# Kernel tuning notes

Hardware: AMD Instinct MI355X
Metric: run time of the kernel (lower is better)

The kernel has to match this reference:

```python
import jax, jax.numpy as jnp
import numpy as np
from jax import lax

NUM_PATCHES = 64   # FPS sample count K
PATCH_SIZE = 32    # KNN neighbors per patch


def setup_inputs() -> dict:
    key = jax.random.key(0)
    points = jax.random.normal(key, (16, 65536, 3), dtype=jnp.float32)
    return {"points": points}


def _fps(xyz, K):
    """Iterative farthest point sampling. xyz: [B,N,3] -> idx [B,K].
    Deterministic start at index 0 (reference for random_start_point)."""
    B, N, _ = xyz.shape
    start = jnp.zeros((B,), dtype=jnp.int32)
    min_d0 = jnp.full((B, N), jnp.finfo(xyz.dtype).max, xyz.dtype)

    def step(carry, _):
        min_d, last = carry
        last_pt = jnp.take_along_axis(xyz, last[:, None, None], axis=1)  # [B,1,3]
        d = jnp.sum((xyz - last_pt) ** 2, axis=-1)                       # [B,N]
        min_d = jnp.minimum(min_d, d)
        nxt = jnp.argmax(min_d, axis=1).astype(jnp.int32)
        return (min_d, nxt), last

    (_, _), idxs = lax.scan(step, (min_d0, start), None, length=K)  # [K,B]
    return jnp.transpose(idxs)  # [B,K]


def _knn_idx(centers, pts, K):
    """K nearest neighbors (sorted ascending by distance). centers [B,P,3], pts [B,N,3]."""
    c2 = jnp.sum(centers * centers, -1)[:, :, None]                 # [B,P,1]
    p2 = jnp.sum(pts * pts, -1)[:, None, :]                         # [B,1,N]
    d2 = c2 + p2 - 2.0 * jnp.einsum('bpc,bnc->bpn', centers, pts)   # [B,P,N]
    _, idx = lax.top_k(-d2, K)                                      # sorted nearest-first
    return idx


def reference(points):
    xyz = points[..., :3]
    fps_idx = _fps(xyz, NUM_PATCHES)                                  # [B,P]
    centers = jnp.take_along_axis(xyz, fps_idx[..., None], axis=1)    # [B,P,3]
    idx = _knn_idx(centers, xyz, PATCH_SIZE)                          # [B,P,K]
    patches = jax.vmap(lambda p, i: p[i])(points, idx)                # [B,P,K,C]
    patches = patches.at[..., :3].add(-centers[:, :, None, :])        # center xyz part
    return patches, centers
```

## Files before the change

### kernel.cpp

```cpp
#include <hip/hip_runtime.h>
#include <float.h>

#define BATCH 16
#define NPTS  65536
#define NP    64
#define PS    32
#define SLICES 8
#define SLICE_PTS (NPTS / SLICES)
#define CAP   192


__device__ __forceinline__ unsigned long long enc64(double d) {
    unsigned long long u = (unsigned long long)__double_as_longlong(d);
    return u ^ ((u >> 63) ? 0xFFFFFFFFFFFFFFFFull : 0x8000000000000000ull);
}
__device__ __forceinline__ unsigned enc32(float f) {
    unsigned u = __float_as_uint(f);
    return u ^ ((u >> 31) ? 0xFFFFFFFFu : 0x80000000u);
}
__device__ __forceinline__ float dec32(unsigned e) {
    unsigned u = (e & 0x80000000u) ? (e ^ 0x80000000u) : ~e;
    return __uint_as_float(u);
}

#define SENT 0xFFFFFFFFFFFFFFFFull

__global__ __launch_bounds__(256, 2)
void fps_kernel(const float* __restrict__ pts,
                float* __restrict__ centers,
                unsigned long long* __restrict__ slots)
{
#pragma clang fp contract(off)
    const int b  = blockIdx.x & 15;
    const int wg = blockIdx.x >> 4;
    const int t  = threadIdx.x;
    const float* __restrict__ P = pts + (size_t)b * NPTS * 3;

    float x[16], y[16], z[16];
    double md[16];
    const int gi0 = wg * 4096 + t;
#pragma unroll
    for (int k = 0; k < 16; ++k) {
        int i = gi0 + (k << 8);
        x[k] = P[3*i+0]; y[k] = P[3*i+1]; z[k] = P[3*i+2];
        md[k] = DBL_MAX;
    }

    double cx = (double)P[0], cy = (double)P[1], cz = (double)P[2];
    if (wg == 0 && t == 0) {
        float* c0 = centers + b * (NP*3);
        c0[0] = P[0]; c0[1] = P[1]; c0[2] = P[2];
    }

    __shared__ unsigned long long wbest[4];
    __shared__ unsigned long long skey[16];

    unsigned long long* slot_it = slots + (size_t)b * 63 * 16;

    for (int it = 0; it < NP - 1; ++it) {
        double bd = -1.0; int bi = 0;
#pragma unroll
        for (int k = 0; k < 16; ++k) {
            double dx = (double)x[k] - cx;
            double dy = (double)y[k] - cy;
            double dz = (double)z[k] - cz;
            double d  = (dx*dx + dy*dy) + dz*dz;
            double m  = fmin(md[k], d);
            md[k] = m;
            if (m > bd) { bd = m; bi = gi0 + (k << 8); }
        }
        unsigned long long db  = (unsigned long long)__double_as_longlong(bd);
        unsigned long long key = 0x8000000000000000ull
                               | (db & 0xFFFFFFFFFFFF0000ull)
                               | (unsigned long long)((~bi) & 0xFFFF);
#pragma unroll
        for (int off = 32; off > 0; off >>= 1) {
            unsigned long long o = __shfl_xor(key, off, 64);
            if (o > key) key = o;
        }
        if ((t & 63) == 0) wbest[t >> 6] = key;
        __syncthreads();
        if (t == 0) {
            unsigned long long k0 = wbest[0];
            if (wbest[1] > k0) k0 = wbest[1];
            if (wbest[2] > k0) k0 = wbest[2];
            if (wbest[3] > k0) k0 = wbest[3];
            __hip_atomic_store(slot_it + wg, k0, __ATOMIC_RELAXED, __HIP_MEMORY_SCOPE_AGENT);
        }
        if (t < 16) {
            unsigned long long v;
            v = __hip_atomic_load(slot_it + t, __ATOMIC_RELAXED, __HIP_MEMORY_SCOPE_AGENT);
            while (v == 0) {
                __builtin_amdgcn_s_sleep(1);
                v = __hip_atomic_load(slot_it + t, __ATOMIC_RELAXED, __HIP_MEMORY_SCOPE_AGENT);
            }
            skey[t] = v;
        }
        __syncthreads();
        unsigned long long bk = skey[0];
#pragma unroll
        for (int j = 1; j < 16; ++j) if (skey[j] > bk) bk = skey[j];
        int sel = (int)((~bk) & 0xFFFFull);
        cx = (double)P[3*sel+0]; cy = (double)P[3*sel+1]; cz = (double)P[3*sel+2];
        if (wg == 0 && t == 0) {
            float* c = centers + b*(NP*3) + (it+1)*3;
            c[0] = P[3*sel+0]; c[1] = P[3*sel+1]; c[2] = P[3*sel+2];
        }
        slot_it += 16;
    }
}

__global__ __launch_bounds__(256, 4)
void knn_pass(const float* __restrict__ pts,
              const float* __restrict__ centers,
              unsigned long long* __restrict__ gkeys)
{
    const int t    = threadIdx.x;
    const int lane = t & 63;
    const int wid  = t >> 6;
    const int b    = blockIdx.x & 15;
    const int w    = (blockIdx.x >> 4) & 15;
    const int s    = blockIdx.x >> 8;
    const float* __restrict__ P = pts + (size_t)b * NPTS * 3;
    const int sbase = s * SLICE_PTS;
    const float4* __restrict__ P4 = (const float4*)(P + 3 * sbase);

    float m2x[4], m2y[4], m2z[4], c2f[4];
#pragma unroll
    for (int g = 0; g < 4; ++g) {
        int c = b * NP + w * 4 + g;
        float cx = centers[3*c+0], cy = centers[3*c+1], cz = centers[3*c+2];
        c2f[g] = cx*cx + cy*cy + cz*cz;
        m2x[g] = -2.0f*cx; m2y[g] = -2.0f*cy; m2z[g] = -2.0f*cz;
    }

    union PoolKeys {
        unsigned pool[4][512];
        unsigned long long keys[4][CAP];
    };
    __shared__ PoolKeys pk;
    __shared__ float    theta4[4];
    __shared__ int      cnt4[4];
    __shared__ unsigned idxbuf[4][CAP];

    float s0[4], s1[4];
#pragma unroll
    for (int g = 0; g < 4; ++g) { s0[g] = FLT_MAX; s1[g] = FLT_MAX; }
    {
        float4 A = P4[3*t], B = P4[3*t+1], C = P4[3*t+2];
        for (int k = 0; k < SLICE_PTS/1024; ++k) {
            int vb = ((k+1) & 7)*768 + 3*t;
            float4 An = P4[vb], Bn = P4[vb+1], Cn = P4[vb+2];
            float qx[4] = {A.x, A.w, B.z, C.y};
            float qy[4] = {A.y, B.x, B.w, C.z};
            float qz[4] = {A.z, B.y, C.x, C.w};
#pragma unroll
            for (int j = 0; j < 4; ++j) {
                float px = qx[j], py = qy[j], pz = qz[j];
                float p2 = px*px + py*py + pz*pz;
#pragma unroll
                for (int g = 0; g < 4; ++g) {
                    float d2 = fmaf(m2x[g], px, fmaf(m2y[g], py, fmaf(m2z[g], pz, c2f[g]))) + p2;
                    s1[g] = __builtin_amdgcn_fmed3f(s0[g], s1[g], d2);
                    s0[g] = fminf(s0[g], d2);
                }
            }
            A = An; B = Bn; C = Cn;
        }
    }
#pragma unroll
    for (int g = 0; g < 4; ++g) {
        pk.pool[g][t]       = enc32(s0[g]);
        pk.pool[g][256 + t] = enc32(s1[g]);
    }
    if (t < 4) cnt4[t] = 0;
    __syncthreads();

    {
        const int g = wid;
        unsigned e[8];
#pragma unroll
        for (int j = 0; j < 8; ++j) e[j] = pk.pool[g][lane * 8 + j];
        unsigned ans = 0;
        for (int bit = 31; bit >= 0; --bit) {
            unsigned test = ans | ((1u << bit) - 1u);
            int cnt = 0;
#pragma unroll
            for (int j = 0; j < 8; ++j)
                cnt += (int)__popcll(__ballot(e[j] <= test));
            if (cnt < 32) ans |= (1u << bit);
        }
        if (lane == 0) theta4[g] = dec32(ans) + 4.0e-3f;
    }
    __syncthreads();
    float th[4];
#pragma unroll
    for (int g = 0; g < 4; ++g) th[g] = theta4[g];

    {
        float4 A = P4[3*t], B = P4[3*t+1], C = P4[3*t+2];
        for (int k = 0; k < SLICE_PTS/1024; ++k) {
            int vb = ((k+1) & 7)*768 + 3*t;
            float4 An = P4[vb], Bn = P4[vb+1], Cn = P4[vb+2];
            float qx[4] = {A.x, A.w, B.z, C.y};
            float qy[4] = {A.y, B.x, B.w, C.z};
            float qz[4] = {A.z, B.y, C.x, C.w};
            int ib = sbase + (k << 10) + (t << 2);
#pragma unroll
            for (int j = 0; j < 4; ++j) {
                float px = qx[j], py = qy[j], pz = qz[j];
                float p2 = px*px + py*py + pz*pz;
#pragma unroll
                for (int g = 0; g < 4; ++g) {
                    float d2 = fmaf(m2x[g], px, fmaf(m2y[g], py, fmaf(m2z[g], pz, c2f[g]))) + p2;
                    if (d2 <= th[g]) {
                        int pos = atomicAdd(&cnt4[g], 1);
                        if (pos < CAP) idxbuf[g][pos] = (unsigned)(ib + j);
                    }
                }
            }
            A = An; B = Bn; C = Cn;
        }
    }
    __syncthreads();

    {
        const int g = wid;
        int n = cnt4[g]; if (n > CAP) n = CAP;
        double cxd, cyd, czd, c2d;
        {
#pragma clang fp contract(off)
            cxd = -0.5*(double)m2x[g]; cyd = -0.5*(double)m2y[g]; czd = -0.5*(double)m2z[g];
            c2d = (cxd*cxd + cyd*cyd) + czd*czd;
        }
        unsigned long long rg[3];
#pragma unroll
        for (int j = 0; j < 3; ++j) {
            int p_ = lane + 64*j;
            if (p_ < n) {
                unsigned i = idxbuf[g][p_];
                double d2x;
                {
#pragma clang fp contract(off)
                    double px_ = (double)P[3*i+0];
                    double py_ = (double)P[3*i+1];
                    double pz_ = (double)P[3*i+2];
                    double p2_ = (px_*px_ + py_*py_) + pz_*pz_;
                    double dt_ = (cxd*px_ + cyd*py_) + czd*pz_;
                    d2x = (c2d + p2_) - 2.0*dt_;
                }
                rg[j] = (enc64(d2x) & 0xFFFFFFFFFFFF0000ull)
                      | (unsigned long long)(i & 0xFFFF);
                pk.keys[g][p_] = rg[j];
            } else rg[j] = SENT;
        }
        const int c = b * NP + w * 4 + g;
        int rank0 = 0, rank1 = 0, rank2 = 0;
        for (int p = 0; p < n; ++p) {
            unsigned long long kj = pk.keys[g][p];
            rank0 += (kj < rg[0]);
            rank1 += (kj < rg[1]);
            rank2 += (kj < rg[2]);
        }
        unsigned long long* gout = gkeys + ((size_t)c * SLICES + s) * PS;
        if (lane       < n && rank0 < PS) gout[rank0] = rg[0];
        if (lane + 64  < n && rank1 < PS) gout[rank1] = rg[1];
        if (lane + 128 < n && rank2 < PS) gout[rank2] = rg[2];
    }
}

__global__ __launch_bounds__(256, 4)
void knn_merge(const float* __restrict__ pts,
               const float* __restrict__ centers,
               const unsigned long long* __restrict__ gkeys,
               float* __restrict__ patches)
{
    const int lane = threadIdx.x & 63;
    const int wid  = threadIdx.x >> 6;
    const int b    = blockIdx.x & 15;
    const int grp  = blockIdx.x >> 4;
    const int c    = b * NP + grp * 4 + wid;
    const float* __restrict__ P = pts + (size_t)b * NPTS * 3;

    unsigned long long rg[4];
#pragma unroll
    for (int j = 0; j < 4; ++j)
        rg[j] = gkeys[(size_t)c * (SLICES*PS) + j*64 + lane];

    unsigned long long okey = SENT;
    for (int r = 0; r < PS; ++r) {
        unsigned long long mn = rg[0]; int mp = 0;
        if (rg[1] < mn) { mn = rg[1]; mp = 1; }
        if (rg[2] < mn) { mn = rg[2]; mp = 2; }
        if (rg[3] < mn) { mn = rg[3]; mp = 3; }
        unsigned long long wm = mn;
#pragma unroll
        for (int off = 32; off > 0; off >>= 1) {
            unsigned long long o = __shfl_xor(wm, off, 64);
            if (o < wm) wm = o;
        }
        if (wm == mn) {
            if (mp == 0) rg[0] = SENT;
            else if (mp == 1) rg[1] = SENT;
            else if (mp == 2) rg[2] = SENT;
            else rg[3] = SENT;
        }
        if (lane == r) okey = wm;
    }

    const float cx = centers[3*c+0], cy = centers[3*c+1], cz = centers[3*c+2];
    if (lane < PS) {
        int i = (int)(okey & 0xFFFFull);
        float* o = patches + (((size_t)c * PS) + lane) * 3;
        o[0] = P[3*i+0] - cx;
        o[1] = P[3*i+1] - cy;
        o[2] = P[3*i+2] - cz;
    }
}

extern "C" void kernel_launch(void* const* d_in, const int* in_sizes, int n_in,
                              void* d_out, int out_size, void* d_ws, size_t ws_size,
                              hipStream_t stream)
{
    const float* pts = (const float*)d_in[0];
    float* out      = (float*)d_out;
    float* patches  = out;
    float* centers  = out + (size_t)BATCH*NP*PS*3;

    unsigned long long* slots = (unsigned long long*)d_ws;
    unsigned long long* gkeys = (unsigned long long*)((char*)d_ws + 131072);

    (void)hipMemsetAsync(d_ws, 0, (size_t)BATCH * 63 * 16 * sizeof(unsigned long long), stream);
    fps_kernel<<<dim3(256), dim3(256), 0, stream>>>(pts, centers, slots);
    knn_pass<<<dim3(2048), dim3(256), 0, stream>>>(pts, centers, gkeys);
    knn_merge<<<dim3(256), dim3(256), 0, stream>>>(pts, centers, gkeys, patches);
}
```

Baseline: 224.0 us.

## Halve KNN slices and replace merge tournament with rank-based placement

Cuts the number of point slices per center from 8 to 4, so each knn_pass block scans twice as many points and the grid launches half as many blocks. The per-slice candidate cap grows to 256, and the exact double-precision ranking covers four keys per lane. The merge kernel drops the 32-round shuffle-min tournament and instead ranks 128 candidates by counting through shared memory, writing each top-32 key straight to its output position. The threshold pool is also read in a strided, lane-contiguous order. The trade is fewer blocks and less parallelism in the scan pass against a shorter merge and less candidate traffic.

```diff
diff --git a/kernel.cpp b/kernel.cpp
--- a/kernel.cpp
+++ b/kernel.cpp
@@ -5,9 +5,9 @@
 #define NPTS  65536
 #define NP    64
 #define PS    32
-#define SLICES 8
+#define SLICES 4
 #define SLICE_PTS (NPTS / SLICES)
-#define CAP   192
+#define CAP   256
 
 
 __device__ __forceinline__ unsigned long long enc64(double d) {
@@ -149,7 +149,7 @@
     {
         float4 A = P4[3*t], B = P4[3*t+1], C = P4[3*t+2];
         for (int k = 0; k < SLICE_PTS/1024; ++k) {
-            int vb = ((k+1) & 7)*768 + 3*t;
+            int vb = ((k+1) & 15)*768 + 3*t;
             float4 An = P4[vb], Bn = P4[vb+1], Cn = P4[vb+2];
             float qx[4] = {A.x, A.w, B.z, C.y};
             float qy[4] = {A.y, B.x, B.w, C.z};
@@ -180,7 +180,7 @@
         const int g = wid;
         unsigned e[8];
 #pragma unroll
-        for (int j = 0; j < 8; ++j) e[j] = pk.pool[g][lane * 8 + j];
+        for (int j = 0; j < 8; ++j) e[j] = pk.pool[g][j * 64 + lane];
         unsigned ans = 0;
         for (int bit = 31; bit >= 0; --bit) {
             unsigned test = ans | ((1u << bit) - 1u);
@@ -200,7 +200,7 @@
     {
         float4 A = P4[3*t], B = P4[3*t+1], C = P4[3*t+2];
         for (int k = 0; k < SLICE_PTS/1024; ++k) {
-            int vb = ((k+1) & 7)*768 + 3*t;
+            int vb = ((k+1) & 15)*768 + 3*t;
             float4 An = P4[vb], Bn = P4[vb+1], Cn = P4[vb+2];
             float qx[4] = {A.x, A.w, B.z, C.y};
             float qy[4] = {A.y, B.x, B.w, C.z};
@@ -233,9 +233,9 @@
             cxd = -0.5*(double)m2x[g]; cyd = -0.5*(double)m2y[g]; czd = -0.5*(double)m2z[g];
             c2d = (cxd*cxd + cyd*cyd) + czd*czd;
         }
-        unsigned long long rg[3];
-#pragma unroll
-        for (int j = 0; j < 3; ++j) {
+        unsigned long long rg[4];
+#pragma unroll
+        for (int j = 0; j < 4; ++j) {
             int p_ = lane + 64*j;
             if (p_ < n) {
                 unsigned i = idxbuf[g][p_];
@@ -255,17 +255,18 @@
             } else rg[j] = SENT;
         }
         const int c = b * NP + w * 4 + g;
-        int rank0 = 0, rank1 = 0, rank2 = 0;
+        int rk[4] = {0, 0, 0, 0};
         for (int p = 0; p < n; ++p) {
             unsigned long long kj = pk.keys[g][p];
-            rank0 += (kj < rg[0]);
-            rank1 += (kj < rg[1]);
-            rank2 += (kj < rg[2]);
+            rk[0] += (kj < rg[0]);
+            rk[1] += (kj < rg[1]);
+            rk[2] += (kj < rg[2]);
+            rk[3] += (kj < rg[3]);
         }
         unsigned long long* gout = gkeys + ((size_t)c * SLICES + s) * PS;
-        if (lane       < n && rank0 < PS) gout[rank0] = rg[0];
-        if (lane + 64  < n && rank1 < PS) gout[rank1] = rg[1];
-        if (lane + 128 < n && rank2 < PS) gout[rank2] = rg[2];
+#pragma unroll
+        for (int j = 0; j < 4; ++j)
+            if (lane + 64*j < n && rk[j] < PS) gout[rk[j]] = rg[j];
     }
 }
 
@@ -282,36 +283,32 @@
     const int c    = b * NP + grp * 4 + wid;
     const float* __restrict__ P = pts + (size_t)b * NPTS * 3;
 
-    unsigned long long rg[4];
-#pragma unroll
-    for (int j = 0; j < 4; ++j)
-        rg[j] = gkeys[(size_t)c * (SLICES*PS) + j*64 + lane];
-
-    unsigned long long okey = SENT;
-    for (int r = 0; r < PS; ++r) {
-        unsigned long long mn = rg[0]; int mp = 0;
-        if (rg[1] < mn) { mn = rg[1]; mp = 1; }
-        if (rg[2] < mn) { mn = rg[2]; mp = 2; }
-        if (rg[3] < mn) { mn = rg[3]; mp = 3; }
-        unsigned long long wm = mn;
-#pragma unroll
-        for (int off = 32; off > 0; off >>= 1) {
-            unsigned long long o = __shfl_xor(wm, off, 64);
-            if (o < wm) wm = o;
-        }
-        if (wm == mn) {
-            if (mp == 0) rg[0] = SENT;
-            else if (mp == 1) rg[1] = SENT;
-            else if (mp == 2) rg[2] = SENT;
-            else rg[3] = SENT;
-        }
-        if (lane == r) okey = wm;
+    __shared__ unsigned long long mk[4][SLICES*PS];
+
+    unsigned long long rg0 = gkeys[(size_t)c * (SLICES*PS) + lane];
+    unsigned long long rg1 = gkeys[(size_t)c * (SLICES*PS) + 64 + lane];
+    mk[wid][lane]      = rg0;
+    mk[wid][64 + lane] = rg1;
+
+    int r0 = 0, r1 = 0;
+#pragma unroll 4
+    for (int p = 0; p < SLICES*PS; ++p) {
+        unsigned long long kj = mk[wid][p];
+        r0 += (kj < rg0);
+        r1 += (kj < rg1);
     }
 
     const float cx = centers[3*c+0], cy = centers[3*c+1], cz = centers[3*c+2];
-    if (lane < PS) {
-        int i = (int)(okey & 0xFFFFull);
-        float* o = patches + (((size_t)c * PS) + lane) * 3;
+    if (r0 < PS) {
+        int i = (int)(rg0 & 0xFFFFull);
+        float* o = patches + (((size_t)c * PS) + r0) * 3;
+        o[0] = P[3*i+0] - cx;
+        o[1] = P[3*i+1] - cy;
+        o[2] = P[3*i+2] - cz;
+    }
+    if (r1 < PS) {
+        int i = (int)(rg1 & 0xFFFFull);
+        float* o = patches + (((size_t)c * PS) + r1) * 3;
         o[0] = P[3*i+0] - cx;
         o[1] = P[3*i+1] - cy;
         o[2] = P[3*i+2] - cz;
@@ -332,6 +329,6 @@
 
     (void)hipMemsetAsync(d_ws, 0, (size_t)BATCH * 63 * 16 * sizeof(unsigned long long), stream);
     fps_kernel<<<dim3(256), dim3(256), 0, stream>>>(pts, centers, slots);
-    knn_pass<<<dim3(2048), dim3(256), 0, stream>>>(pts, centers, gkeys);
+    knn_pass<<<dim3(1024), dim3(256), 0, stream>>>(pts, centers, gkeys);
     knn_merge<<<dim3(256), dim3(256), 0, stream>>>(pts, centers, gkeys, patches);
 }
```

New measurement: 212.1 us. 1.06x faster.
